# Performance work log

Measured on AMD Instinct MI355X. Metric: run time of the kernel, lower is better.

## Reference

```python
import jax, jax.numpy as jnp
import numpy as np
import math

NPASS = 10
B = 16384
IN_DIM = 2048
C = 101
PI = 0.5
SIGMA1 = 1.0            # exp(-0)
SIGMA2 = math.exp(-6.0)
LOG_SQRT_2PI = 0.5 * math.log(2.0 * math.pi)


def setup_inputs() -> dict:
    key = jax.random.key(0)
    ks = jax.random.split(key, 7)
    x = jax.random.normal(ks[0], (B, IN_DIM), jnp.float32)
    weight_mu = jax.random.uniform(ks[1], (C, IN_DIM), jnp.float32, -0.2, 0.2)
    weight_rho = jax.random.uniform(ks[2], (C, IN_DIM), jnp.float32, -5.0, -4.0)
    bias_mu = jax.random.uniform(ks[3], (C,), jnp.float32, -0.2, 0.2)
    bias_rho = jax.random.uniform(ks[4], (C,), jnp.float32, -5.0, -4.0)
    eps_w = jax.random.normal(ks[5], (NPASS, C, IN_DIM), jnp.float32)
    eps_b = jax.random.normal(ks[6], (NPASS, C), jnp.float32)
    return {"x": x, "weight_mu": weight_mu, "weight_rho": weight_rho,
            "bias_mu": bias_mu, "bias_rho": bias_rho,
            "eps_w": eps_w, "eps_b": eps_b, "npass": NPASS}


def _mixture_log_prob(v, axes):
    # log( pi*N(v;0,s1) + (1-pi)*N(v;0,s2) ), summed over param axes (per pass)
    lp1 = -LOG_SQRT_2PI - math.log(SIGMA1) - v * v / (2.0 * SIGMA1 ** 2)
    lp2 = -LOG_SQRT_2PI - math.log(SIGMA2) - v * v / (2.0 * SIGMA2 ** 2)
    return jnp.log(PI * jnp.exp(lp1) + (1.0 - PI) * jnp.exp(lp2)).sum(axes)


def _posterior_log_prob(v, mu, sigma, axes):
    return (-LOG_SQRT_2PI - jnp.log(sigma)
            - (v - mu) ** 2 / (2.0 * sigma ** 2)).sum(axes)


def reference(x, weight_mu, weight_rho, bias_mu, bias_rho, eps_w, eps_b, npass):
    # Reparameterized Gaussian sampling (vectorized over npass)
    sigma_w = jnp.log1p(jnp.exp(weight_rho))        # [C, I]
    sigma_b = jnp.log1p(jnp.exp(bias_rho))          # [C]
    w = weight_mu + sigma_w * eps_w                 # [n, C, I]
    b = bias_mu + sigma_b * eps_b                   # [n, C]

    # outputs[i] = x @ w[i].T + b[i]  -> [n, B, C]
    outputs = jnp.einsum('bi,noi->nbo', x, w) + b[:, None, :]
    pred_mean = outputs.mean(0)                     # [B, C]

    # scale-mixture prior and variational posterior log-probs, per pass
    log_priors = _mixture_log_prob(w, (1, 2)) + _mixture_log_prob(b, (1,))
    log_posts = (_posterior_log_prob(w, weight_mu, sigma_w, (1, 2))
                 + _posterior_log_prob(b, bias_mu, sigma_b, (1,)))
    log_prior = log_priors.mean()
    log_posterior = log_posts.mean()

    p = jax.nn.softmax(outputs, axis=-1)            # [n, B, C]
    # trace(diag(p) - p p^T) = sum(p) - sum(p^2) ; avoids [n,B,C,C] outer products
    aleatoric = (p.sum(-1) - (p * p).sum(-1)).mean(0)   # [B]
    p_bar = p.mean(0)                                   # [B, C]
    # trace((p - p_bar)(p - p_bar)^T) = sum((p - p_bar)^2)
    epistemic = ((p - p_bar) ** 2).sum(-1).mean(0)      # [B]

    return pred_mean, log_prior, log_posterior, aleatoric, epistemic
```

## Files before the change

### kernel.cpp

```cpp
#include <hip/hip_runtime.h>
#include <hip/hip_bf16.h>
#include <math.h>

#define NB    16384
#define KDIM  2048
#define NCLS  101
#define NP    10
#define NTOT  (NP*NCLS)
#define NPAD  1024
#define PM_SIZE (NB*NCLS)
#define CI    (NCLS*KDIM)
#define NBLK_PW ((CI + 255) / 256)
#define PAD_ELEMS ((NPAD - NTOT) * KDIM)

#define LSQ2PI 0.9189385332046727f
#define HALF_INV_S2SQ 81377.39570642986f

typedef __bf16 bf16x8 __attribute__((ext_vector_type(8)));
typedef float f32x4 __attribute__((ext_vector_type(4)));

__device__ __forceinline__ unsigned short f2bf_bits(float f) {
    union { float f; unsigned u; } v; v.f = f;
    unsigned u = v.u;
    unsigned r = u + 0x7FFFu + ((u >> 16) & 1u);
    return (unsigned short)(r >> 16);
}

__device__ __forceinline__ bf16x8 cvt8(float4 a, float4 b) {
    bf16x8 r;
    r[0] = (__bf16)a.x; r[1] = (__bf16)a.y; r[2] = (__bf16)a.z; r[3] = (__bf16)a.w;
    r[4] = (__bf16)b.x; r[5] = (__bf16)b.y; r[6] = (__bf16)b.z; r[7] = (__bf16)b.w;
    return r;
}

__device__ __forceinline__ float mix_logprob(float v) {
    float q = v * v;
    float lp1 = -LSQ2PI - 0.5f * q;
    float lp2 = -LSQ2PI + 6.0f - HALF_INV_S2SQ * q;
    return __logf(0.5f * __expf(lp1) + 0.5f * __expf(lp2));
}

__global__ void prep_weights(const float* __restrict__ wmu, const float* __restrict__ wrho,
                             const float* __restrict__ eps_w,
                             unsigned short* __restrict__ wB, float* __restrict__ partials) {
    const int t = blockIdx.x * 256 + threadIdx.x;
    if (t < PAD_ELEMS) wB[(size_t)NTOT * KDIM + t] = 0;
    float prior = 0.f, post = 0.f;
    if (t < CI) {
        const float mu = wmu[t];
        const float sigma = log1pf(__expf(wrho[t]));
        const float nls = -__logf(sigma);
        const int c = t / KDIM, i = t & (KDIM - 1);
        #pragma unroll
        for (int n = 0; n < NP; ++n) {
            const float eps = eps_w[(size_t)n * CI + t];
            const float w = fmaf(sigma, eps, mu);
            wB[(size_t)(n * NCLS + c) * KDIM + i] = f2bf_bits(w);
            prior += mix_logprob(w);
            post += nls - LSQ2PI - 0.5f * eps * eps;
        }
    }
    for (int off = 32; off; off >>= 1) {
        prior += __shfl_xor(prior, off);
        post  += __shfl_xor(post, off);
    }
    __shared__ float sp[4], so[4];
    const int wid = threadIdx.x >> 6;
    if ((threadIdx.x & 63) == 0) { sp[wid] = prior; so[wid] = post; }
    __syncthreads();
    if (threadIdx.x == 0) {
        partials[blockIdx.x * 2]     = sp[0] + sp[1] + sp[2] + sp[3];
        partials[blockIdx.x * 2 + 1] = so[0] + so[1] + so[2] + so[3];
    }
}

__global__ void prep_bias(const float* __restrict__ bmu, const float* __restrict__ brho,
                          const float* __restrict__ eps_b, const float* __restrict__ partials,
                          float* __restrict__ biasN, float* __restrict__ out) {
    const int t = threadIdx.x;
    float prior = 0.f, post = 0.f, bv = 0.f;
    if (t < NTOT) {
        const int c = t % NCLS;
        const float sigma = log1pf(__expf(brho[c]));
        const float eps = eps_b[t];
        bv = fmaf(sigma, eps, bmu[c]);
        prior = mix_logprob(bv);
        post = -LSQ2PI - __logf(sigma) - 0.5f * eps * eps;
    }
    biasN[t] = bv;
    if (t < NBLK_PW) { prior += partials[2 * t]; post += partials[2 * t + 1]; }
    for (int off = 32; off; off >>= 1) {
        prior += __shfl_xor(prior, off);
        post  += __shfl_xor(post, off);
    }
    __shared__ float sp[16], so[16];
    const int wid = t >> 6;
    if ((t & 63) == 0) { sp[wid] = prior; so[wid] = post; }
    __syncthreads();
    if (t == 0) {
        float a = 0.f, b = 0.f;
        for (int i = 0; i < 16; ++i) { a += sp[i]; b += so[i]; }
        out[PM_SIZE]     = a * (1.0f / NP);
        out[PM_SIZE + 1] = b * (1.0f / NP);
    }
}

__device__ __forceinline__ void stage_half(const unsigned short* __restrict__ G,
                                           int grow0, int k0, int lds_byte_base,
                                           int tid, char* ldsp) {
    #pragma unroll
    for (int l = 0; l < 2; ++l) {
        const int flat = l * 512 + tid;
        const int row = flat >> 3, j = flat & 7;
        const int jsw = j ^ (row & 7);
        const unsigned short* src = G + (size_t)(grow0 + row) * KDIM + k0 + jsw * 8;
        __builtin_amdgcn_global_load_lds(
            (const __attribute__((address_space(1))) void*)src,
            (__attribute__((address_space(3))) void*)(ldsp + lds_byte_base + flat * 16),
            16, 0, 0);
    }
}

#define STAGE_B(buf, half, tt) stage_half(Bm, bn + (half) * 128, (tt) * 64, ((buf) * 4 + 2 + (half)) * 16384, tid, ldsp)

#define A_LOAD(dst, half, tt) do { \
    const float* p0_ = X + (size_t)(bm + (half) * 128 + ar0) * KDIM + (tt) * 64 + ac0; \
    const float* p1_ = X + (size_t)(bm + (half) * 128 + ar1) * KDIM + (tt) * 64 + ac1; \
    dst[0] = *(const float4*)p0_; dst[1] = *(const float4*)(p0_ + 4); \
    dst[2] = *(const float4*)p1_; dst[3] = *(const float4*)(p1_ + 4); \
} while (0)

#define A_WRITE(src, half, buf_) do { \
    char* base_ = ldsp + (((buf_) * 4 + (half)) * 16384); \
    *(bf16x8*)(base_ + aw0) = cvt8(src[0], src[1]); \
    *(bf16x8*)(base_ + aw1) = cvt8(src[2], src[3]); \
} while (0)

#define LDA(mf, buf) do { \
    const int rowh_ = (mf) * 16 + l15; \
    const char* p_ = ldsp + ((buf) * 4 + aregion) * 16384 + rowh_ * 128; \
    const int sw_ = (rowh_ & 7) << 4; \
    af[(mf) & 3][0] = *(const bf16x8*)(p_ + ((l4 << 4) ^ sw_)); \
    af[(mf) & 3][1] = *(const bf16x8*)(p_ + (((4 + l4) << 4) ^ sw_)); \
} while (0)

#define LDB(nf, buf) do { \
    const int rowh_ = (wc & 1) * 64 + (nf) * 16 + l15; \
    const char* p_ = ldsp + ((buf) * 4 + bregion) * 16384 + rowh_ * 128; \
    const int sw_ = (rowh_ & 7) << 4; \
    bf[nf][0] = *(const bf16x8*)(p_ + ((l4 << 4) ^ sw_)); \
    bf[nf][1] = *(const bf16x8*)(p_ + (((4 + l4) << 4) ^ sw_)); \
} while (0)

#define MM(mh, nh) do { \
    __builtin_amdgcn_s_setprio(1); \
    _Pragma("unroll") \
    for (int mi = 0; mi < 4; ++mi) \
        _Pragma("unroll") \
        for (int ni = 0; ni < 2; ++ni) \
            _Pragma("unroll") \
            for (int kk = 0; kk < 2; ++kk) \
                acc[(mh) * 4 + mi][(nh) * 2 + ni] = __builtin_amdgcn_mfma_f32_16x16x32_bf16( \
                    af[mi][kk], bf[(nh) * 2 + ni][kk], acc[(mh) * 4 + mi][(nh) * 2 + ni], 0, 0, 0); \
    __builtin_amdgcn_s_setprio(0); \
} while (0)

#define SBAR() do { \
    __builtin_amdgcn_sched_barrier(0); \
    __builtin_amdgcn_s_barrier(); \
    __builtin_amdgcn_sched_barrier(0); \
} while (0)

__global__ void __launch_bounds__(512, 2) gemm8(
    const float* __restrict__ X,
    const unsigned short* __restrict__ Bm,
    const float* __restrict__ biasN,
    float* __restrict__ Cout)
{
    __shared__ __align__(16) unsigned short lds[65536];
    char* ldsp = (char*)lds;
    const int tid = threadIdx.x;
    const int lane = tid & 63, wid = tid >> 6;
    const int wr = wid >> 2, wc = wid & 3;
    const int l15 = lane & 15, l4 = lane >> 4;

    const int b = blockIdx.x;
    const int wg = (b & 7) * 32 + (b >> 3);
    const int bm = (wg >> 2) * 256;
    const int bn = (wg & 3) * 256;

    const int aregion = wr;
    const int bregion = 2 + (wc >> 1);

    const int s0 = tid * 2, s1 = s0 + 1;
    const int ar0 = s0 >> 3, ac0 = (s0 & 7) * 8;
    const int ar1 = s1 >> 3, ac1 = (s1 & 7) * 8;
    const int aw0 = ar0 * 128 + (((s0 & 7) ^ (ar0 & 7)) << 4);
    const int aw1 = ar1 * 128 + (((s1 & 7) ^ (ar1 & 7)) << 4);

    f32x4 acc[8][4] = {{}};
    bf16x8 af[4][2], bf[4][2];
    float4 aH0[4], aH1[4];

    A_LOAD(aH1, 1, 0);
    A_LOAD(aH0, 0, 0);
    STAGE_B(0, 0, 0); STAGE_B(0, 1, 0);
    STAGE_B(1, 0, 1); STAGE_B(1, 1, 1);
    __builtin_amdgcn_sched_barrier(0);
    asm volatile("s_waitcnt vmcnt(8)");
    __builtin_amdgcn_sched_barrier(0);
    A_WRITE(aH1, 1, 0);
    A_WRITE(aH0, 0, 0);
    __builtin_amdgcn_sched_barrier(0);
    asm volatile("s_waitcnt vmcnt(4) lgkmcnt(0)");
    __builtin_amdgcn_s_barrier();
    __builtin_amdgcn_sched_barrier(0);

    for (int t = 0; t < 32; ++t) {
        const int buf = t & 1, nbuf = buf ^ 1;
        const bool pf = (t + 1 < 32);
        LDA(0, buf); LDA(1, buf); LDA(2, buf); LDA(3, buf);
        LDB(0, buf); LDB(1, buf);
        if (pf) { A_LOAD(aH1, 1, t + 1); A_LOAD(aH0, 0, t + 1); }
        SBAR();
        MM(0, 0);
        SBAR();
        LDB(2, buf); LDB(3, buf);
        SBAR();
        MM(0, 1);
        SBAR();
        LDA(4, buf); LDA(5, buf); LDA(6, buf); LDA(7, buf);
        if (t + 2 < 32) STAGE_B(buf, 0, t + 2);
        __builtin_amdgcn_sched_barrier(0);
        if (t < 30) { asm volatile("s_waitcnt vmcnt(6)"); }
        else        { asm volatile("s_waitcnt vmcnt(0)"); }
        __builtin_amdgcn_sched_barrier(0);
        if (pf) A_WRITE(aH1, 1, nbuf);
        SBAR();
        MM(1, 1);
        SBAR();
        if (t + 2 < 32) STAGE_B(buf, 1, t + 2);
        __builtin_amdgcn_sched_barrier(0);
        if (t < 30) { asm volatile("s_waitcnt vmcnt(4)"); }
        else        { asm volatile("s_waitcnt vmcnt(0)"); }
        __builtin_amdgcn_sched_barrier(0);
        if (pf) A_WRITE(aH0, 0, nbuf);
        SBAR();
        MM(1, 0);
        __builtin_amdgcn_sched_barrier(0);
        asm volatile("s_waitcnt lgkmcnt(0)");
        __builtin_amdgcn_s_barrier();
        __builtin_amdgcn_sched_barrier(0);
    }

    #pragma unroll
    for (int n = 0; n < 4; ++n) {
        const int col = bn + wc * 64 + n * 16 + l15;
        const float bv = biasN[col];
        #pragma unroll
        for (int m = 0; m < 8; ++m) {
            const int row0 = bm + wr * 128 + m * 16 + l4 * 4;
            #pragma unroll
            for (int r = 0; r < 4; ++r)
                Cout[(size_t)(row0 + r) * NPAD + col] = acc[m][n][r] + bv;
        }
    }
}

__global__ void stats_kernel(const float* __restrict__ Cout, float* __restrict__ out) {
    const int lane = threadIdx.x & 63;
    const int wid = threadIdx.x >> 6;
    const int b = blockIdx.x * 4 + wid;
    const float* row = Cout + (size_t)b * NPAD;
    float* pm = out;
    float* aleat_out = out + PM_SIZE + 2;
    float* epi_out   = out + PM_SIZE + 2 + NB;

    const bool has2 = lane < (NCLS - 64);
    float p1s[NP], p2s[NP];
    float pm1 = 0.f, pm2 = 0.f, pb1 = 0.f, pb2 = 0.f, aleat = 0.f;

    for (int n = 0; n < NP; ++n) {
        const float v1 = row[n * NCLS + lane];
        const float v2 = has2 ? row[n * NCLS + 64 + lane] : -INFINITY;
        float mx = fmaxf(v1, v2);
        for (int off = 32; off; off >>= 1) mx = fmaxf(mx, __shfl_xor(mx, off));
        const float e1 = __expf(v1 - mx);
        const float e2 = has2 ? __expf(v2 - mx) : 0.f;
        float s = e1 + e2;
        for (int off = 32; off; off >>= 1) s += __shfl_xor(s, off);
        const float p1 = e1 / s, p2 = e2 / s;
        float spp = p1 + p2, sq = p1 * p1 + p2 * p2;
        for (int off = 32; off; off >>= 1) {
            spp += __shfl_xor(spp, off);
            sq  += __shfl_xor(sq, off);
        }
        aleat += spp - sq;
        pm1 += v1; pm2 += v2;
        pb1 += p1; pb2 += p2;
        p1s[n] = p1; p2s[n] = p2;
    }
    const float inv_n = 1.0f / NP;
    pb1 *= inv_n; pb2 *= inv_n;
    pm[(size_t)b * NCLS + lane] = pm1 * inv_n;
    if (has2) pm[(size_t)b * NCLS + 64 + lane] = pm2 * inv_n;
    float epi = 0.f;
    #pragma unroll
    for (int n = 0; n < NP; ++n) {
        const float d1 = p1s[n] - pb1;
        const float d2 = p2s[n] - pb2;
        epi += d1 * d1 + d2 * d2;
    }
    for (int off = 32; off; off >>= 1) epi += __shfl_xor(epi, off);
    if (lane == 0) {
        aleat_out[b] = aleat * inv_n;
        epi_out[b]   = epi * inv_n;
    }
}

extern "C" void kernel_launch(void* const* d_in, const int* in_sizes, int n_in,
                              void* d_out, int out_size, void* d_ws, size_t ws_size,
                              hipStream_t stream) {
    const float* x     = (const float*)d_in[0];
    const float* wmu   = (const float*)d_in[1];
    const float* wrho  = (const float*)d_in[2];
    const float* bmu   = (const float*)d_in[3];
    const float* brho  = (const float*)d_in[4];
    const float* eps_w = (const float*)d_in[5];
    const float* eps_b = (const float*)d_in[6];
    float* out = (float*)d_out;

    char* ws = (char*)d_ws;
    const size_t OFF_WB    = 0;
    const size_t OFF_COUT  = OFF_WB + 4194304;
    const size_t OFF_BIASN = OFF_COUT + 67108864;
    const size_t OFF_PART  = OFF_BIASN + 4096;

    unsigned short* wB   = (unsigned short*)(ws + OFF_WB);
    float* Cout     = (float*)(ws + OFF_COUT);
    float* biasN    = (float*)(ws + OFF_BIASN);
    float* partials = (float*)(ws + OFF_PART);

    prep_weights<<<NBLK_PW, 256, 0, stream>>>(wmu, wrho, eps_w, wB, partials);
    prep_bias<<<1, 1024, 0, stream>>>(bmu, brho, eps_b, partials, biasN, out);
    gemm8<<<256, 512, 0, stream>>>(x, wB, biasN, Cout);
    stats_kernel<<<NB / 4, 256, 0, stream>>>(Cout, out);
}
```

Measured before the change: 149.2 us.

## Halve GEMM M-tile to 128 rows and prefetch A two tiles ahead

The GEMM block tile shrinks from 256x256 to 128x256 and the grid doubles to 512 blocks, which fills the 256 CUs more evenly and cuts the per-block accumulator registers. LDS use drops to 96KB, and the A operand (fp32 x converted to bf16) is now register-prefetched two k-steps ahead using alternating register sets, with the loop unrolled by two. The cost is lower arithmetic intensity per block, so B weights are reloaded twice as often.

```diff
diff --git a/kernel.cpp b/kernel.cpp
--- a/kernel.cpp
+++ b/kernel.cpp
@@ -12,6 +12,7 @@
 #define CI    (NCLS*KDIM)
 #define NBLK_PW ((CI + 255) / 256)
 #define PAD_ELEMS ((NPAD - NTOT) * KDIM)
+#define NT    32
 
 #define LSQ2PI 0.9189385332046727f
 #define HALF_INV_S2SQ 81377.39570642986f
@@ -121,53 +122,85 @@
     }
 }
 
-#define STAGE_B(buf, half, tt) stage_half(Bm, bn + (half) * 128, (tt) * 64, ((buf) * 4 + 2 + (half)) * 16384, tid, ldsp)
-
-#define A_LOAD(dst, half, tt) do { \
-    const float* p0_ = X + (size_t)(bm + (half) * 128 + ar0) * KDIM + (tt) * 64 + ac0; \
-    const float* p1_ = X + (size_t)(bm + (half) * 128 + ar1) * KDIM + (tt) * 64 + ac1; \
-    dst[0] = *(const float4*)p0_; dst[1] = *(const float4*)(p0_ + 4); \
-    dst[2] = *(const float4*)p1_; dst[3] = *(const float4*)(p1_ + 4); \
-} while (0)
-
-#define A_WRITE(src, half, buf_) do { \
-    char* base_ = ldsp + (((buf_) * 4 + (half)) * 16384); \
-    *(bf16x8*)(base_ + aw0) = cvt8(src[0], src[1]); \
-    *(bf16x8*)(base_ + aw1) = cvt8(src[2], src[3]); \
+#define STAGE_B2(buf, tt) do { \
+    stage_half(Bm, bn,       (tt) * 64, 32768 + (buf) * 32768,         tid, ldsp); \
+    stage_half(Bm, bn + 128, (tt) * 64, 32768 + (buf) * 32768 + 16384, tid, ldsp); \
+} while (0)
+
+#define A_LOAD(SET, tt) do { \
+    const float* p_ = X + (size_t)(bm + arow) * KDIM + (tt) * 64 + acol; \
+    SET[0] = *(const float4*)p_;        SET[1] = *(const float4*)(p_ + 4); \
+    SET[2] = *(const float4*)(p_ + 8);  SET[3] = *(const float4*)(p_ + 12); \
+} while (0)
+
+#define A_WRITE(SET, dstbuf) do { \
+    char* base_ = ldsp + (dstbuf) * 16384; \
+    *(bf16x8*)(base_ + aw0) = cvt8(SET[0], SET[1]); \
+    *(bf16x8*)(base_ + aw1) = cvt8(SET[2], SET[3]); \
 } while (0)
 
 #define LDA(mf, buf) do { \
-    const int rowh_ = (mf) * 16 + l15; \
-    const char* p_ = ldsp + ((buf) * 4 + aregion) * 16384 + rowh_ * 128; \
-    const int sw_ = (rowh_ & 7) << 4; \
-    af[(mf) & 3][0] = *(const bf16x8*)(p_ + ((l4 << 4) ^ sw_)); \
-    af[(mf) & 3][1] = *(const bf16x8*)(p_ + (((4 + l4) << 4) ^ sw_)); \
+    const int row_ = wr * 64 + (mf) * 16 + l15; \
+    const char* p_ = ldsp + (buf) * 16384 + row_ * 128; \
+    const int sw_ = (row_ & 7) << 4; \
+    af[mf][0] = *(const bf16x8*)(p_ + ((l4 << 4) ^ sw_)); \
+    af[mf][1] = *(const bf16x8*)(p_ + (((4 + l4) << 4) ^ sw_)); \
 } while (0)
 
 #define LDB(nf, buf) do { \
-    const int rowh_ = (wc & 1) * 64 + (nf) * 16 + l15; \
-    const char* p_ = ldsp + ((buf) * 4 + bregion) * 16384 + rowh_ * 128; \
-    const int sw_ = (rowh_ & 7) << 4; \
+    const int row_ = (wc & 1) * 64 + (nf) * 16 + l15; \
+    const char* p_ = ldsp + 32768 + (buf) * 32768 + (wc >> 1) * 16384 + row_ * 128; \
+    const int sw_ = (row_ & 7) << 4; \
     bf[nf][0] = *(const bf16x8*)(p_ + ((l4 << 4) ^ sw_)); \
     bf[nf][1] = *(const bf16x8*)(p_ + (((4 + l4) << 4) ^ sw_)); \
 } while (0)
 
-#define MM(mh, nh) do { \
+#define MM(mp, np) do { \
     __builtin_amdgcn_s_setprio(1); \
     _Pragma("unroll") \
-    for (int mi = 0; mi < 4; ++mi) \
+    for (int mi = 0; mi < 2; ++mi) \
         _Pragma("unroll") \
         for (int ni = 0; ni < 2; ++ni) \
             _Pragma("unroll") \
             for (int kk = 0; kk < 2; ++kk) \
-                acc[(mh) * 4 + mi][(nh) * 2 + ni] = __builtin_amdgcn_mfma_f32_16x16x32_bf16( \
-                    af[mi][kk], bf[(nh) * 2 + ni][kk], acc[(mh) * 4 + mi][(nh) * 2 + ni], 0, 0, 0); \
+                acc[(mp) * 2 + mi][(np) * 2 + ni] = __builtin_amdgcn_mfma_f32_16x16x32_bf16( \
+                    af[(mp) * 2 + mi][kk], bf[(np) * 2 + ni][kk], acc[(mp) * 2 + mi][(np) * 2 + ni], 0, 0, 0); \
     __builtin_amdgcn_s_setprio(0); \
 } while (0)
 
 #define SBAR() do { \
     __builtin_amdgcn_sched_barrier(0); \
     __builtin_amdgcn_s_barrier(); \
+    __builtin_amdgcn_sched_barrier(0); \
+} while (0)
+
+#define TILE(t, buf, LSET, WSET) do { \
+     \
+    LDA(0, buf); LDA(1, buf); \
+    LDB(0, buf); LDB(1, buf); \
+    if ((t) < NT - 2) { A_LOAD(LSET, (t) + 2); } \
+    SBAR(); \
+    MM(0, 0); \
+    SBAR(); \
+     \
+    LDB(2, buf); LDB(3, buf); \
+    SBAR(); \
+    MM(0, 1); \
+    SBAR(); \
+     \
+    LDA(2, buf); LDA(3, buf); \
+    __builtin_amdgcn_sched_barrier(0); \
+    if ((t) < NT - 2)        { asm volatile("s_waitcnt vmcnt(8)"); } \
+    else if ((t) == NT - 2)  { asm volatile("s_waitcnt vmcnt(4)"); } \
+    __builtin_amdgcn_sched_barrier(0); \
+    if ((t) < NT - 1) { A_WRITE(WSET, (buf) ^ 1); } \
+    if ((t) < NT - 2) { STAGE_B2(buf, (t) + 2); } \
+    SBAR(); \
+    MM(1, 1); \
+    MM(1, 0); \
+    __builtin_amdgcn_sched_barrier(0); \
+    if ((t) < NT - 2)        { asm volatile("s_waitcnt vmcnt(8) lgkmcnt(0)"); __builtin_amdgcn_s_barrier(); } \
+    else if ((t) == NT - 2)  { asm volatile("s_waitcnt vmcnt(0) lgkmcnt(0)"); __builtin_amdgcn_s_barrier(); } \
     __builtin_amdgcn_sched_barrier(0); \
 } while (0)
 
@@ -177,7 +210,7 @@
     const float* __restrict__ biasN,
     float* __restrict__ Cout)
 {
-    __shared__ __align__(16) unsigned short lds[65536];
+    __shared__ __align__(16) unsigned short lds[49152];
     char* ldsp = (char*)lds;
     const int tid = threadIdx.x;
     const int lane = tid & 63, wid = tid >> 6;
@@ -185,72 +218,38 @@
     const int l15 = lane & 15, l4 = lane >> 4;
 
     const int b = blockIdx.x;
-    const int wg = (b & 7) * 32 + (b >> 3);
-    const int bm = (wg >> 2) * 256;
+    const int wg = (b & 7) * 64 + (b >> 3);
+    const int bm = (wg >> 2) * 128;
     const int bn = (wg & 3) * 256;
 
-    const int aregion = wr;
-    const int bregion = 2 + (wc >> 1);
-
-    const int s0 = tid * 2, s1 = s0 + 1;
-    const int ar0 = s0 >> 3, ac0 = (s0 & 7) * 8;
-    const int ar1 = s1 >> 3, ac1 = (s1 & 7) * 8;
-    const int aw0 = ar0 * 128 + (((s0 & 7) ^ (ar0 & 7)) << 4);
-    const int aw1 = ar1 * 128 + (((s1 & 7) ^ (ar1 & 7)) << 4);
-
-    f32x4 acc[8][4] = {{}};
+    const int arow = tid >> 2;
+    const int acol = (tid & 3) * 16;
+    const int j0 = (2 * tid) & 7, j1 = j0 + 1;
+    const int aw0 = arow * 128 + ((j0 ^ (arow & 7)) << 4);
+    const int aw1 = arow * 128 + ((j1 ^ (arow & 7)) << 4);
+
+    f32x4 acc[4][4] = {{}};
     bf16x8 af[4][2], bf[4][2];
-    float4 aH0[4], aH1[4];
-
-    A_LOAD(aH1, 1, 0);
-    A_LOAD(aH0, 0, 0);
-    STAGE_B(0, 0, 0); STAGE_B(0, 1, 0);
-    STAGE_B(1, 0, 1); STAGE_B(1, 1, 1);
+    float4 aR0[4], aR1[4];
+
+    A_LOAD(aR0, 0);
+    STAGE_B2(0, 0);
+    A_LOAD(aR1, 1);
+    STAGE_B2(1, 1);
     __builtin_amdgcn_sched_barrier(0);
-    asm volatile("s_waitcnt vmcnt(8)");
+    asm volatile("s_waitcnt vmcnt(12)");
     __builtin_amdgcn_sched_barrier(0);
-    A_WRITE(aH1, 1, 0);
-    A_WRITE(aH0, 0, 0);
+    A_WRITE(aR0, 0);
     __builtin_amdgcn_sched_barrier(0);
-    asm volatile("s_waitcnt vmcnt(4) lgkmcnt(0)");
+    asm volatile("s_waitcnt vmcnt(8) lgkmcnt(0)");
     __builtin_amdgcn_s_barrier();
     __builtin_amdgcn_sched_barrier(0);
 
-    for (int t = 0; t < 32; ++t) {
-        const int buf = t & 1, nbuf = buf ^ 1;
-        const bool pf = (t + 1 < 32);
-        LDA(0, buf); LDA(1, buf); LDA(2, buf); LDA(3, buf);
-        LDB(0, buf); LDB(1, buf);
-        if (pf) { A_LOAD(aH1, 1, t + 1); A_LOAD(aH0, 0, t + 1); }
-        SBAR();
-        MM(0, 0);
-        SBAR();
-        LDB(2, buf); LDB(3, buf);
-        SBAR();
-        MM(0, 1);
-        SBAR();
-        LDA(4, buf); LDA(5, buf); LDA(6, buf); LDA(7, buf);
-        if (t + 2 < 32) STAGE_B(buf, 0, t + 2);
-        __builtin_amdgcn_sched_barrier(0);
-        if (t < 30) { asm volatile("s_waitcnt vmcnt(6)"); }
-        else        { asm volatile("s_waitcnt vmcnt(0)"); }
-        __builtin_amdgcn_sched_barrier(0);
-        if (pf) A_WRITE(aH1, 1, nbuf);
-        SBAR();
-        MM(1, 1);
-        SBAR();
-        if (t + 2 < 32) STAGE_B(buf, 1, t + 2);
-        __builtin_amdgcn_sched_barrier(0);
-        if (t < 30) { asm volatile("s_waitcnt vmcnt(4)"); }
-        else        { asm volatile("s_waitcnt vmcnt(0)"); }
-        __builtin_amdgcn_sched_barrier(0);
-        if (pf) A_WRITE(aH0, 0, nbuf);
-        SBAR();
-        MM(1, 0);
-        __builtin_amdgcn_sched_barrier(0);
-        asm volatile("s_waitcnt lgkmcnt(0)");
-        __builtin_amdgcn_s_barrier();
-        __builtin_amdgcn_sched_barrier(0);
+    #pragma unroll 1
+    for (int tt = 0; tt < NT / 2; ++tt) {
+        const int t0 = 2 * tt;
+        TILE(t0,     0, aR0, aR1);
+        TILE(t0 + 1, 1, aR1, aR0);
     }
 
     #pragma unroll
@@ -258,8 +257,8 @@
         const int col = bn + wc * 64 + n * 16 + l15;
         const float bv = biasN[col];
         #pragma unroll
-        for (int m = 0; m < 8; ++m) {
-            const int row0 = bm + wr * 128 + m * 16 + l4 * 4;
+        for (int m = 0; m < 4; ++m) {
+            const int row0 = bm + wr * 64 + m * 16 + l4 * 4;
             #pragma unroll
             for (int r = 0; r < 4; ++r)
                 Cout[(size_t)(row0 + r) * NPAD + col] = acc[m][n][r] + bv;
@@ -343,6 +342,6 @@
 
     prep_weights<<<NBLK_PW, 256, 0, stream>>>(wmu, wrho, eps_w, wB, partials);
     prep_bias<<<1, 1024, 0, stream>>>(bmu, brho, eps_b, partials, biasN, out);
-    gemm8<<<256, 512, 0, stream>>>(x, wB, biasN, Cout);
+    gemm8<<<512, 512, 0, stream>>>(x, wB, biasN, Cout);
     stats_kernel<<<NB / 4, 256, 0, stream>>>(Cout, out);
 }
```

Measured after the change: 145.0 us. -2.9%, faster.
